# Performance work log

Hardware: AMD Instinct MI355X
Metric: run time of the kernel (lower is better)

The kernel has to match this reference:

```python
import jax, jax.numpy as jnp
import numpy as np
from jax import lax

B, N = 16, 4096


def _fps(xyz, npoint):
    # xyz: [N,3] -> [npoint] int32 indices (iterative farthest point sampling, start at idx 0)
    n = xyz.shape[0]
    def step(carry, _):
        dist, far = carry
        d = jnp.sum((xyz - xyz[far]) ** 2, axis=-1)
        dist = jnp.minimum(dist, d)
        nxt = jnp.argmax(dist).astype(jnp.int32)
        return (dist, nxt), far
    (_, _), idx = lax.scan(step, (jnp.full((n,), 1e10, xyz.dtype), jnp.int32(0)), None, length=npoint)
    return idx


def _ball_query(xyz, new_xyz, radius, nsample):
    # xyz: [N,3], new_xyz: [S,3] -> [S, nsample] neighbor indices within radius
    n = xyz.shape[0]
    sqr = jnp.sum((new_xyz[:, None, :] - xyz[None, :, :]) ** 2, axis=-1)  # [S,N]
    idx = jnp.where(sqr > radius * radius, n, jnp.arange(n)[None, :])
    idx = jnp.sort(idx, axis=-1)[:, :nsample]
    return jnp.where(idx == n, idx[:, :1], idx)  # pad misses with first hit


def _gather(p, i):
    return p[i]


def _mlp(feat, ws):
    # feat: [B,S,K,C]; 1x1 conv + folded eval-BN + ReLU per layer
    for W, b in ws:
        feat = jax.nn.relu(jnp.einsum('bskc,oc->bsko', feat, W) + b)
    return feat


def _sa(xyz, points, npoint, radius, nsample, ws):
    fps_idx = jax.vmap(_fps, in_axes=(0, None))(xyz, npoint)              # [B,S]
    new_xyz = jnp.take_along_axis(xyz, fps_idx[..., None], axis=1)         # [B,S,3]
    idx = jax.vmap(_ball_query, in_axes=(0, 0, None, None))(xyz, new_xyz, radius, nsample)  # [B,S,K]
    grouped_xyz = jax.vmap(_gather)(xyz, idx) - new_xyz[:, :, None, :]     # [B,S,K,3]
    if points is None:
        feat = grouped_xyz
    else:
        feat = jnp.concatenate([grouped_xyz, jax.vmap(_gather)(points, idx)], axis=-1)
    return new_xyz, jnp.max(_mlp(feat, ws), axis=2)                        # [B,S,Cout]


def _forward(x, ws1, ws2, ws3, fw, fb):
    b = x.shape[0]
    l1_xyz, l1_pts = _sa(x, None, 512, 0.2, 32, ws1)       # [B,512,3], [B,512,128]
    l2_xyz, l2_pts = _sa(l1_xyz, l1_pts, 128, 0.4, 64, ws2)  # [B,128,3], [B,128,256]
    feat = jnp.concatenate([l2_xyz, l2_pts], axis=-1)[:, None]  # group_all: [B,1,128,259]
    g = jnp.max(_mlp(feat, ws3), axis=2).reshape(b, 1024)
    return g @ fw.T + fb


_SPECS = [
    ('sa1_w0', (64, 3)), ('sa1_b0', (64,)), ('sa1_w1', (64, 64)), ('sa1_b1', (64,)), ('sa1_w2', (128, 64)), ('sa1_b2', (128,)),
    ('sa2_w0', (128, 131)), ('sa2_b0', (128,)), ('sa2_w1', (128, 128)), ('sa2_b1', (128,)), ('sa2_w2', (256, 128)), ('sa2_b2', (256,)),
    ('sa3_w0', (256, 259)), ('sa3_b0', (256,)), ('sa3_w1', (512, 256)), ('sa3_b1', (512,)), ('sa3_w2', (1024, 512)), ('sa3_b2', (1024,)),
    ('fw', (1024, 1024)), ('fb', (1024,)),
]


def setup_inputs() -> dict:
    key = jax.random.key(0)
    keys = jax.random.split(key, len(_SPECS) + 1)
    inp = {'x': jax.random.uniform(keys[0], (B, N, 3), dtype=jnp.float32)}
    for (name, shp), k in zip(_SPECS, keys[1:]):
        inp[name] = jax.random.normal(k, shp, dtype=jnp.float32) * 0.02
    return inp


def reference(x, sa1_w0, sa1_b0, sa1_w1, sa1_b1, sa1_w2, sa1_b2,
              sa2_w0, sa2_b0, sa2_w1, sa2_b1, sa2_w2, sa2_b2,
              sa3_w0, sa3_b0, sa3_w1, sa3_b1, sa3_w2, sa3_b2, fw, fb):
    ws1 = [(sa1_w0, sa1_b0), (sa1_w1, sa1_b1), (sa1_w2, sa1_b2)]
    ws2 = [(sa2_w0, sa2_b0), (sa2_w1, sa2_b1), (sa2_w2, sa2_b2)]
    ws3 = [(sa3_w0, sa3_b0), (sa3_w1, sa3_b1), (sa3_w2, sa3_b2)]
    return _forward(x, ws1, ws2, ws3, fw, fb)
```

## Files before the change

### kernel.cpp

```cpp
#include <hip/hip_runtime.h>

#ifndef BATCH
#define BATCH 16
#endif

typedef float f32x2 __attribute__((ext_vector_type(2)));
__device__ __forceinline__ f32x2 mk2(float a, float b) { f32x2 r; r.x = a; r.y = b; return r; }

template<int CTRL>
__device__ __forceinline__ float dppmaxf(float v)
{
    const int d = __builtin_amdgcn_update_dpp(__float_as_int(v), __float_as_int(v),
                                              CTRL, 0xf, 0xf, false);
    return fmaxf(v, __int_as_float(d));
}
template<int CTRL>
__device__ __forceinline__ unsigned dppminu(unsigned v)
{
    const unsigned d = (unsigned)__builtin_amdgcn_update_dpp((int)v, (int)v,
                                                             CTRL, 0xf, 0xf, false);
    return (d < v) ? d : v;
}
__device__ __forceinline__ float wave_max_bcast(float v)
{
    v = dppmaxf<0x111>(v);
    v = dppmaxf<0x112>(v);
    v = dppmaxf<0x114>(v);
    v = dppmaxf<0x118>(v);
    v = dppmaxf<0x142>(v);
    v = dppmaxf<0x143>(v);
    return __int_as_float(__builtin_amdgcn_readlane(__float_as_int(v), 63));
}
__device__ __forceinline__ unsigned wave_min_bcast(unsigned v)
{
    v = dppminu<0x111>(v);
    v = dppminu<0x112>(v);
    v = dppminu<0x114>(v);
    v = dppminu<0x118>(v);
    v = dppminu<0x142>(v);
    v = dppminu<0x143>(v);
    return (unsigned)__builtin_amdgcn_readlane((int)v, 63);
}

__device__ __forceinline__ void transpose_body(int blk, int tid,
    const float* __restrict__ s0, float* __restrict__ d0,
    const float* __restrict__ s1, float* __restrict__ d1,
    const float* __restrict__ s2, float* __restrict__ d2,
    const float* __restrict__ s3, float* __restrict__ d3,
    const float* __restrict__ s4, float* __restrict__ d4,
    const float* __restrict__ s5, float* __restrict__ d5,
    const float* __restrict__ s6, float* __restrict__ d6,
    const float* __restrict__ s7, float* __restrict__ d7,
    const float* __restrict__ s8, float* __restrict__ d8)
{
    int i = blk * 256 + tid;
    if (i < 192)    { d0[(i%3)  *64   + i/3  ] = s0[i]; return; }  i -= 192;
    if (i < 4096)   { d1[(i&63) *64   + (i>>6)] = s1[i]; return; } i -= 4096;
    if (i < 8192)   { d2[(i&63) *128  + (i>>6)] = s2[i]; return; } i -= 8192;
    if (i < 16768)  { d3[(i%131)*128  + i/131] = s3[i]; return; }  i -= 16768;
    if (i < 16384)  { d4[(i&127)*128  + (i>>7)] = s4[i]; return; } i -= 16384;
    if (i < 32768)  { d5[(i&127)*256  + (i>>7)] = s5[i]; return; } i -= 32768;
    if (i < 66304)  { d6[(i%259)*256  + i/259] = s6[i]; return; }  i -= 66304;
    if (i < 131072) { d7[(i&255)*512  + (i>>8)] = s7[i]; return; } i -= 131072;
    if (i < 524288) { d8[(i&511)*1024 + (i>>9)] = s8[i]; return; }
}

template<int N, int NP1, int NP2, int BLOCK>
__global__ __launch_bounds__(BLOCK)
void fps_fused(const float* __restrict__ xyz,
               float* __restrict__ out1, float* __restrict__ out2,
               const float* __restrict__ ts0, float* __restrict__ td0,
               const float* __restrict__ ts1, float* __restrict__ td1,
               const float* __restrict__ ts2, float* __restrict__ td2,
               const float* __restrict__ ts3, float* __restrict__ td3,
               const float* __restrict__ ts4, float* __restrict__ td4,
               const float* __restrict__ ts5, float* __restrict__ td5,
               const float* __restrict__ ts6, float* __restrict__ td6,
               const float* __restrict__ ts7, float* __restrict__ td7,
               const float* __restrict__ ts8, float* __restrict__ td8)
{
#pragma clang fp contract(off)
    if ((int)blockIdx.x >= BATCH) {
        transpose_body(blockIdx.x - BATCH, threadIdx.x,
                       ts0, td0, ts1, td1, ts2, td2, ts3, td3, ts4, td4,
                       ts5, td5, ts6, td6, ts7, td7, ts8, td8);
        return;
    }
    constexpr int P  = N / BLOCK;
    constexpr int P2 = NP1 / BLOCK;
    constexpr int NW = BLOCK / 64;
    __shared__ float sx[N], sy[N], sz[N];
    __shared__ float s2x[NP1], s2y[NP1], s2z[NP1];
    __shared__ float o2x[NP2], o2y[NP2], o2z[NP2];
    __shared__ unsigned long long wslot[2][NW];
    const int b = blockIdx.x, t = threadIdx.x;
    const int lane = t & 63, wv = t >> 6;
    const float* xb = xyz + (size_t)b * N * 3;
    float px[P], py[P], pz[P], dist[P];
#pragma unroll
    for (int j = 0; j < P; ++j) {
        const int i = t + j * BLOCK;
        const float x = xb[i*3+0], y = xb[i*3+1], z = xb[i*3+2];
        sx[i] = x; sy[i] = y; sz[i] = z;
        px[j] = x; py[j] = y; pz[j] = z;
        dist[j] = 1e10f;
    }
    __syncthreads();
    float fx = sx[0], fy = sy[0], fz = sz[0];
    if (t == 0) { s2x[0] = fx; s2y[0] = fy; s2z[0] = fz; }
    for (int s = 1; s < NP1; ++s) {
        float bestv = -1.f; int besti = 0;
#pragma unroll
        for (int j = 0; j < P; ++j) {
            const float dx = px[j]-fx, dy = py[j]-fy, dz = pz[j]-fz;
            const float d = (dx*dx + dy*dy) + dz*dz;
            const float nd = fminf(dist[j], d);
            dist[j] = nd;
            if (nd > bestv) { bestv = nd; besti = t + j * BLOCK; }
        }
        const float wm = wave_max_bcast(bestv);
        const unsigned cand = (bestv == wm) ? (unsigned)besti : 0xffffffffu;
        const unsigned wi = wave_min_bcast(cand);
        const int par = s & 1;
        if (lane == 0)
            wslot[par][wv] = ((unsigned long long)__float_as_uint(wm) << 32)
                           | (unsigned)(~wi);
        __syncthreads();
        unsigned long long pa = wslot[par][0];
#pragma unroll
        for (int w = 1; w < NW; ++w) {
            const unsigned long long pb = wslot[par][w];
            pa = (pb > pa) ? pb : pa;
        }
        const int far = (int)(~(unsigned)pa);
        fx = sx[far]; fy = sy[far]; fz = sz[far];
        if (t == 0) { s2x[s] = fx; s2y[s] = fy; s2z[s] = fz; }
    }
    __syncthreads();
    float mx[P2], my[P2], mz[P2], d2[P2];
#pragma unroll
    for (int j = 0; j < P2; ++j) {
        const int i = t + j * BLOCK;
        mx[j] = s2x[i]; my[j] = s2y[i]; mz[j] = s2z[i];
        d2[j] = 1e10f;
    }
    fx = s2x[0]; fy = s2y[0]; fz = s2z[0];
    if (t == 0) { o2x[0] = fx; o2y[0] = fy; o2z[0] = fz; }
    for (int s = 1; s < NP2; ++s) {
        float bestv = -1.f; int besti = 0;
#pragma unroll
        for (int j = 0; j < P2; ++j) {
            const float dx = mx[j]-fx, dy = my[j]-fy, dz = mz[j]-fz;
            const float d = (dx*dx + dy*dy) + dz*dz;
            const float nd = fminf(d2[j], d);
            d2[j] = nd;
            if (nd > bestv) { bestv = nd; besti = t + j * BLOCK; }
        }
        const float wm = wave_max_bcast(bestv);
        const unsigned cand = (bestv == wm) ? (unsigned)besti : 0xffffffffu;
        const unsigned wi = wave_min_bcast(cand);
        const int par = s & 1;
        if (lane == 0)
            wslot[par][wv] = ((unsigned long long)__float_as_uint(wm) << 32)
                           | (unsigned)(~wi);
        __syncthreads();
        unsigned long long pa = wslot[par][0];
#pragma unroll
        for (int w = 1; w < NW; ++w) {
            const unsigned long long pb = wslot[par][w];
            pa = (pb > pa) ? pb : pa;
        }
        const int far2 = (int)(~(unsigned)pa);
        fx = s2x[far2]; fy = s2y[far2]; fz = s2z[far2];
        if (t == 0) { o2x[s] = fx; o2y[s] = fy; o2z[s] = fz; }
    }
    __syncthreads();
    for (int i = t; i < NP1; i += BLOCK) {
        out1[((size_t)b*NP1 + i)*3 + 0] = s2x[i];
        out1[((size_t)b*NP1 + i)*3 + 1] = s2y[i];
        out1[((size_t)b*NP1 + i)*3 + 2] = s2z[i];
    }
    for (int i = t; i < NP2; i += BLOCK) {
        out2[((size_t)b*NP2 + i)*3 + 0] = o2x[i];
        out2[((size_t)b*NP2 + i)*3 + 1] = o2y[i];
        out2[((size_t)b*NP2 + i)*3 + 2] = o2z[i];
    }
}

template<int N, int S, int K>
__device__ __forceinline__ void ballq_body(const float* __restrict__ xyz,
                                           const float* __restrict__ nxyz,
                                           int* __restrict__ idx, const float r2,
                                           const int bid, const int tid)
{
#pragma clang fp contract(off)
    const int gw = (bid * 256 + tid) >> 6;
    const int lane = tid & 63;
    const int b = gw / S, s = gw % S;
    const float* xb = xyz + (size_t)b * N * 3;
    const float qx = nxyz[((size_t)b*S + s)*3 + 0];
    const float qy = nxyz[((size_t)b*S + s)*3 + 1];
    const float qz = nxyz[((size_t)b*S + s)*3 + 2];
    int* op = idx + ((size_t)b*S + s) * K;
    int base = 0, first = -1;
    for (int c = 0; c < N; c += 64) {
        const int i = c + lane;
        const float dx = xb[i*3+0]-qx, dy = xb[i*3+1]-qy, dz = xb[i*3+2]-qz;
        const float d = (dx*dx + dy*dy) + dz*dz;
        const bool hit = !(d > r2);
        const unsigned long long m = __ballot(hit);
        if (first < 0 && m) first = c + __builtin_ctzll(m);
        const int pos = base + __popcll(m & ((1ull << lane) - 1ull));
        if (hit && pos < K) op[pos] = i;
        base += __popcll(m);
        if (base >= K) break;
    }
    if (base < K && lane >= base && lane < K) op[lane] = first;
}

__global__ __launch_bounds__(256)
void ballq_both(const float* __restrict__ pts1, const float* __restrict__ q1,
                int* __restrict__ idx1, const float r2a,
                const float* __restrict__ pts2, const float* __restrict__ q2,
                int* __restrict__ idx2, const float r2b)
{
    const int nb1 = (BATCH * 512) / 4;
    if ((int)blockIdx.x < nb1)
        ballq_body<4096, 512, 32>(pts1, q1, idx1, r2a, blockIdx.x, threadIdx.x);
    else
        ballq_body<512, 128, 64>(pts2, q2, idx2, r2b, blockIdx.x - nb1, threadIdx.x);
}

__device__ __forceinline__ void fma16pk(f32x2 (&acc)[8], const float f,
                                        const float* __restrict__ wrow)
{
    const float4 w0 = ((const float4*)wrow)[0];
    const float4 w1 = ((const float4*)wrow)[1];
    const float4 w2 = ((const float4*)wrow)[2];
    const float4 w3 = ((const float4*)wrow)[3];
    const f32x2 ff = mk2(f, f);
    acc[0] += ff * mk2(w0.x, w0.y);
    acc[1] += ff * mk2(w0.z, w0.w);
    acc[2] += ff * mk2(w1.x, w1.y);
    acc[3] += ff * mk2(w1.z, w1.w);
    acc[4] += ff * mk2(w2.x, w2.y);
    acc[5] += ff * mk2(w2.z, w2.w);
    acc[6] += ff * mk2(w3.x, w3.y);
    acc[7] += ff * mk2(w3.z, w3.w);
}

__device__ __forceinline__ float pool_half(float v)
{
    v = fmaxf(v, __shfl_xor(v, 1));
    v = fmaxf(v, __shfl_xor(v, 2));
    v = fmaxf(v, __shfl_xor(v, 4));
    v = fmaxf(v, __shfl_xor(v, 8));
    v = fmaxf(v, __shfl_xor(v, 16));
    return v;
}
__device__ __forceinline__ float pool_full(float v)
{
    v = pool_half(v);
    return fmaxf(v, __shfl_xor(v, 32));
}

__global__ __launch_bounds__(256)
void sa1_fused(const float* __restrict__ xyz, const float* __restrict__ nxyz,
               const int* __restrict__ idx,
               const float* __restrict__ Wt0, const float* __restrict__ B0,
               const float* __restrict__ Wt1, const float* __restrict__ B1,
               const float* __restrict__ Wt2, const float* __restrict__ B2,
               float* __restrict__ out)
{
    __shared__ float buf[64][64];
    const int tid = threadIdx.x, lane = tid & 63;
    const int wave = __builtin_amdgcn_readfirstlane(tid >> 6);
    const int row0 = blockIdx.x * 64;
    const int myrow = row0 + lane;
    const int g = myrow >> 5, b = g >> 9;
    const int i = idx[myrow];
    const float* p = xyz + ((size_t)b*4096 + i) * 3;
    const float f0 = p[0] - nxyz[(size_t)g*3 + 0];
    const float f1 = p[1] - nxyz[(size_t)g*3 + 1];
    const float f2 = p[2] - nxyz[(size_t)g*3 + 2];
    const int oc0 = wave * 16;
    f32x2 aL[8], aH[8];
#pragma unroll
    for (int j = 0; j < 16; ++j) {
        const float v = B0[oc0+j] + f0*Wt0[0*64+oc0+j] + f1*Wt0[1*64+oc0+j] + f2*Wt0[2*64+oc0+j];
        buf[oc0+j][lane] = fmaxf(v, 0.f);
    }
    __syncthreads();
#pragma unroll
    for (int k = 0; k < 8; ++k) aL[k] = mk2(B1[oc0+2*k], B1[oc0+2*k+1]);
#pragma unroll 4
    for (int ci = 0; ci < 64; ++ci)
        fma16pk(aL, buf[ci][lane], Wt1 + ci*64 + oc0);
    __syncthreads();
#pragma unroll
    for (int k = 0; k < 8; ++k) {
        buf[oc0+2*k][lane]   = fmaxf(aL[k].x, 0.f);
        buf[oc0+2*k+1][lane] = fmaxf(aL[k].y, 0.f);
    }
    __syncthreads();
#pragma unroll
    for (int k = 0; k < 8; ++k) {
        aL[k] = mk2(B2[oc0+2*k], B2[oc0+2*k+1]);
        aH[k] = mk2(B2[64+oc0+2*k], B2[64+oc0+2*k+1]);
    }
#pragma unroll 2
    for (int ci = 0; ci < 64; ++ci) {
        const float f = buf[ci][lane];
        fma16pk(aL, f, Wt2 + ci*128 + oc0);
        fma16pk(aH, f, Wt2 + ci*128 + 64 + oc0);
    }
#pragma unroll
    for (int k = 0; k < 8; ++k) {
        const float v0 = pool_half(fmaxf(aL[k].x, 0.f));
        const float v1 = pool_half(fmaxf(aL[k].y, 0.f));
        const float w0 = pool_half(fmaxf(aH[k].x, 0.f));
        const float w1 = pool_half(fmaxf(aH[k].y, 0.f));
        if ((lane & 31) == 0) {
            const size_t orow = (size_t)((row0 + lane) >> 5) * 128;
            out[orow + oc0 + 2*k]       = v0;
            out[orow + oc0 + 2*k + 1]   = v1;
            out[orow + 64 + oc0 + 2*k]     = w0;
            out[orow + 64 + oc0 + 2*k + 1] = w1;
        }
    }
}

__global__ __launch_bounds__(256)
void sa2_fused(const float* __restrict__ l1xyz, const float* __restrict__ l1pts,
               const float* __restrict__ nxyz, const int* __restrict__ idx,
               const float* __restrict__ Wt0, const float* __restrict__ B0,
               const float* __restrict__ Wt1, const float* __restrict__ B1,
               const float* __restrict__ Wt2, const float* __restrict__ B2,
               float* __restrict__ out)
{
    __shared__ float buf[128][64];
    const int tid = threadIdx.x, lane = tid & 63;
    const int wave = __builtin_amdgcn_readfirstlane(tid >> 6);
    const int gblk = blockIdx.x;
    const int b = gblk >> 7;
    const int row0 = gblk * 64;
    const int myi = idx[row0 + lane];
    const float* pc = l1xyz + ((size_t)b*512 + myi) * 3;
    const float f0 = pc[0] - nxyz[(size_t)gblk*3 + 0];
    const float f1 = pc[1] - nxyz[(size_t)gblk*3 + 1];
    const float f2 = pc[2] - nxyz[(size_t)gblk*3 + 2];
    for (int r = wave; r < 64; r += 4) {
        const int i2 = idx[row0 + r];
        const float* src = l1pts + ((size_t)b*512 + i2) * 128;
        buf[lane][r ^ lane]    = src[lane];
        buf[lane+64][r ^ lane] = src[lane + 64];
    }
    __syncthreads();
    const int oc0 = wave * 16;
    f32x2 aL[8], aH[8];
#pragma unroll
    for (int k = 0; k < 8; ++k) {
        const int j0 = oc0 + 2*k, j1 = oc0 + 2*k + 1;
        aL[k] = mk2(B0[j0]    + f0*Wt0[j0]     + f1*Wt0[128+j0]    + f2*Wt0[256+j0],
                    B0[j1]    + f0*Wt0[j1]     + f1*Wt0[128+j1]    + f2*Wt0[256+j1]);
        aH[k] = mk2(B0[64+j0] + f0*Wt0[64+j0]  + f1*Wt0[192+j0]    + f2*Wt0[320+j0],
                    B0[64+j1] + f0*Wt0[64+j1]  + f1*Wt0[192+j1]    + f2*Wt0[320+j1]);
    }
#pragma unroll 2
    for (int ci = 0; ci < 128; ++ci) {
        const float f = buf[ci][lane ^ (ci & 63)];
        const float* wp = Wt0 + (size_t)(ci+3)*128;
        fma16pk(aL, f, wp + oc0);
        fma16pk(aH, f, wp + 64 + oc0);
    }
    __syncthreads();
#pragma unroll
    for (int k = 0; k < 8; ++k) {
        buf[oc0+2*k][lane]      = fmaxf(aL[k].x, 0.f);
        buf[oc0+2*k+1][lane]    = fmaxf(aL[k].y, 0.f);
        buf[64+oc0+2*k][lane]   = fmaxf(aH[k].x, 0.f);
        buf[64+oc0+2*k+1][lane] = fmaxf(aH[k].y, 0.f);
    }
    __syncthreads();
#pragma unroll
    for (int k = 0; k < 8; ++k) {
        aL[k] = mk2(B1[oc0+2*k], B1[oc0+2*k+1]);
        aH[k] = mk2(B1[64+oc0+2*k], B1[64+oc0+2*k+1]);
    }
#pragma unroll 2
    for (int ci = 0; ci < 128; ++ci) {
        const float f = buf[ci][lane];
        const float* wp = Wt1 + (size_t)ci*128;
        fma16pk(aL, f, wp + oc0);
        fma16pk(aH, f, wp + 64 + oc0);
    }
    __syncthreads();
#pragma unroll
    for (int k = 0; k < 8; ++k) {
        buf[oc0+2*k][lane]      = fmaxf(aL[k].x, 0.f);
        buf[oc0+2*k+1][lane]    = fmaxf(aL[k].y, 0.f);
        buf[64+oc0+2*k][lane]   = fmaxf(aH[k].x, 0.f);
        buf[64+oc0+2*k+1][lane] = fmaxf(aH[k].y, 0.f);
    }
    __syncthreads();
    float* orow = out + (size_t)gblk * 256;
    for (int half = 0; half < 2; ++half) {
        const int oc = half*128 + oc0;
#pragma unroll
        for (int k = 0; k < 8; ++k) {
            aL[k] = mk2(B2[oc+2*k], B2[oc+2*k+1]);
            aH[k] = mk2(B2[64+oc+2*k], B2[64+oc+2*k+1]);
        }
#pragma unroll 2
        for (int ci = 0; ci < 128; ++ci) {
            const float f = buf[ci][lane];
            const float* wp = Wt2 + (size_t)ci*256;
            fma16pk(aL, f, wp + oc);
            fma16pk(aH, f, wp + 64 + oc);
        }
#pragma unroll
        for (int k = 0; k < 8; ++k) {
            const float v0 = pool_full(fmaxf(aL[k].x, 0.f));
            const float v1 = pool_full(fmaxf(aL[k].y, 0.f));
            const float w0 = pool_full(fmaxf(aH[k].x, 0.f));
            const float w1 = pool_full(fmaxf(aH[k].y, 0.f));
            if (lane == 0) {
                orow[oc + 2*k]        = v0;
                orow[oc + 2*k + 1]    = v1;
                orow[64 + oc + 2*k]   = w0;
                orow[64 + oc + 2*k+1] = w1;
            }
        }
    }
}

template<int CIN, int COUT, bool CONCAT3, bool POOL>
__global__ __launch_bounds__(256)
void mlp_gemm_kernel(const float* __restrict__ inA, const float* __restrict__ inB,
                     const float* __restrict__ Wt, const float* __restrict__ Bb,
                     float* __restrict__ out)
{
    __shared__ float featS[128][64];
    const int tid = threadIdx.x, lane = tid & 63;
    const int wave = __builtin_amdgcn_readfirstlane(tid >> 6);
    const int row0 = blockIdx.x * 64;
    const int oc0 = blockIdx.y * 64 + wave * 16;
    f32x2 acc[8];
#pragma unroll
    for (int k = 0; k < 8; ++k) acc[k] = mk2(Bb[oc0+2*k], Bb[oc0+2*k+1]);
    for (int c0 = 0; c0 < CIN; c0 += 128) {
        const int csz = (CIN - c0 < 128) ? (CIN - c0) : 128;
        __syncthreads();
        for (int r = wave; r < 64; r += 4) {
            const int row = row0 + r;
            for (int cl = lane; cl < csz; cl += 64) {
                const int cig = c0 + cl;
                float v;
                if (CONCAT3)
                    v = (cig < 3) ? inA[(size_t)row*3 + cig]
                                  : inB[(size_t)row*(CIN-3) + (cig - 3)];
                else
                    v = inA[(size_t)row*CIN + cig];
                featS[cl][r ^ (cl & 63)] = v;
            }
        }
        __syncthreads();
        if (csz == 128) {
#pragma unroll 4
            for (int ci = 0; ci < 128; ++ci)
                fma16pk(acc, featS[ci][lane ^ (ci & 63)], Wt + (size_t)(c0+ci)*COUT + oc0);
        } else {
            for (int ci = 0; ci < csz; ++ci)
                fma16pk(acc, featS[ci][lane ^ (ci & 63)], Wt + (size_t)(c0+ci)*COUT + oc0);
        }
    }
    if (POOL) {
#pragma unroll
        for (int k = 0; k < 8; ++k) {
            const float v0 = pool_full(fmaxf(acc[k].x, 0.f));
            const float v1 = pool_full(fmaxf(acc[k].y, 0.f));
            if (lane == 0) {
                out[(size_t)blockIdx.x * COUT + oc0 + 2*k]     = v0;
                out[(size_t)blockIdx.x * COUT + oc0 + 2*k + 1] = v1;
            }
        }
    } else {
        float4 o0, o1, o2, o3;
        o0.x=fmaxf(acc[0].x,0.f); o0.y=fmaxf(acc[0].y,0.f); o0.z=fmaxf(acc[1].x,0.f); o0.w=fmaxf(acc[1].y,0.f);
        o1.x=fmaxf(acc[2].x,0.f); o1.y=fmaxf(acc[2].y,0.f); o1.z=fmaxf(acc[3].x,0.f); o1.w=fmaxf(acc[3].y,0.f);
        o2.x=fmaxf(acc[4].x,0.f); o2.y=fmaxf(acc[4].y,0.f); o2.z=fmaxf(acc[5].x,0.f); o2.w=fmaxf(acc[5].y,0.f);
        o3.x=fmaxf(acc[6].x,0.f); o3.y=fmaxf(acc[6].y,0.f); o3.z=fmaxf(acc[7].x,0.f); o3.w=fmaxf(acc[7].y,0.f);
        float4* op = (float4*)(out + (size_t)(row0 + lane)*COUT + oc0);
        op[0]=o0; op[1]=o1; op[2]=o2; op[3]=o3;
    }
}

__global__ __launch_bounds__(256)
void fc_kernel(const float* __restrict__ pmax, const float* __restrict__ fw,
               const float* __restrict__ fb, float* __restrict__ y)
{
    const int gw = (blockIdx.x * 256 + threadIdx.x) >> 6;
    const int lane = threadIdx.x & 63;
    const int b = gw >> 10, o = gw & 1023;
    const float4* g0 = (const float4*)(pmax + (size_t)(2*b) * 1024);
    const float4* g1 = (const float4*)(pmax + (size_t)(2*b+1) * 1024);
    const float4* wv = (const float4*)(fw + (size_t)o * 1024);
    float acc = 0.f;
#pragma unroll
    for (int r = 0; r < 4; ++r) {
        const float4 a = g0[lane + r*64];
        const float4 c = g1[lane + r*64];
        const float4 w = wv[lane + r*64];
        acc += fmaxf(a.x,c.x)*w.x + fmaxf(a.y,c.y)*w.y
             + fmaxf(a.z,c.z)*w.z + fmaxf(a.w,c.w)*w.w;
    }
#pragma unroll
    for (int m = 32; m >= 1; m >>= 1) acc += __shfl_xor(acc, m);
    if (lane == 0) y[gw] = acc + fb[o];
}

extern "C" void kernel_launch(void* const* d_in, const int* in_sizes, int n_in,
                              void* d_out, int out_size, void* d_ws, size_t ws_size,
                              hipStream_t stream)
{
    (void)in_sizes; (void)n_in; (void)out_size; (void)ws_size;
    const float* x   = (const float*)d_in[0];
    const float* s1w0 = (const float*)d_in[1];  const float* s1b0 = (const float*)d_in[2];
    const float* s1w1 = (const float*)d_in[3];  const float* s1b1 = (const float*)d_in[4];
    const float* s1w2 = (const float*)d_in[5];  const float* s1b2 = (const float*)d_in[6];
    const float* s2w0 = (const float*)d_in[7];  const float* s2b0 = (const float*)d_in[8];
    const float* s2w1 = (const float*)d_in[9];  const float* s2b1 = (const float*)d_in[10];
    const float* s2w2 = (const float*)d_in[11]; const float* s2b2 = (const float*)d_in[12];
    const float* s3w0 = (const float*)d_in[13]; const float* s3b0 = (const float*)d_in[14];
    const float* s3w1 = (const float*)d_in[15]; const float* s3b1 = (const float*)d_in[16];
    const float* s3w2 = (const float*)d_in[17]; const float* s3b2 = (const float*)d_in[18];
    const float* fw  = (const float*)d_in[19]; const float* fb  = (const float*)d_in[20];
    float* y = (float*)d_out;

    char* ws = (char*)d_ws;
    float* l1_xyz = (float*)(ws + 0);
    int*   idx1   = (int*)  (ws + 98304);
    float* l1_pts = (float*)(ws + 1146880);
    float* l2_xyz = (float*)(ws + 5341184);
    int*   idx2   = (int*)  (ws + 5365760);
    float* l2_pts = (float*)(ws + 5890048);
    float* h1     = (float*)(ws + 7987200);
    float* h2     = (float*)(ws + 10084352);
    float* pmax   = (float*)(ws + 14278656);
    float* wt1_0  = (float*)(ws + 14409728);
    float* wt1_1  = (float*)(ws + 14410496);
    float* wt1_2  = (float*)(ws + 14426880);
    float* wt2_0  = (float*)(ws + 14459648);
    float* wt2_1  = (float*)(ws + 14526720);
    float* wt2_2  = (float*)(ws + 14592256);
    float* wt3_0  = (float*)(ws + 14723328);
    float* wt3_1  = (float*)(ws + 14988544);
    float* wt3_2  = (float*)(ws + 15512832);

    const float r2_1 = (float)(0.2 * 0.2);
    const float r2_2 = (float)(0.4 * 0.4);

    fps_fused<4096, 512, 128, 256><<<BATCH + 3126, 256, 0, stream>>>(
        x, l1_xyz, l2_xyz,
        s1w0, wt1_0, s1w1, wt1_1, s1w2, wt1_2,
        s2w0, wt2_0, s2w1, wt2_1, s2w2, wt2_2,
        s3w0, wt3_0, s3w1, wt3_1, s3w2, wt3_2);
    ballq_both<<<(BATCH*512)/4 + (BATCH*128)/4, 256, 0, stream>>>(
        x, l1_xyz, idx1, r2_1, l1_xyz, l2_xyz, idx2, r2_2);
    sa1_fused<<<(BATCH*512*32)/64, 256, 0, stream>>>(x, l1_xyz, idx1,
        wt1_0, s1b0, wt1_1, s1b1, wt1_2, s1b2, l1_pts);
    sa2_fused<<<BATCH*128, 256, 0, stream>>>(l1_xyz, l1_pts, l2_xyz, idx2,
        wt2_0, s2b0, wt2_1, s2b1, wt2_2, s2b2, l2_pts);
    mlp_gemm_kernel<259, 256,  true,  false><<<dim3(32, 4),  256, 0, stream>>>(l2_xyz, l2_pts, wt3_0, s3b0, h1);
    mlp_gemm_kernel<256, 512,  false, false><<<dim3(32, 8),  256, 0, stream>>>(h1, nullptr, wt3_1, s3b1, h2);
    mlp_gemm_kernel<512, 1024, false, true ><<<dim3(32, 16), 256, 0, stream>>>(h2, nullptr, wt3_2, s3b2, pmax);
    fc_kernel<<<(BATCH*1024)/4, 256, 0, stream>>>(pmax, fw, fb, y);
}
```

Measured before the change: 928.0 us.

## Compute SA1 MLP fully in registers per point, removing shared-memory staging

The SA1 fused MLP is restructured so each thread owns one grouped point and computes all 64/64/128 channels of the three layers in registers. Previously the four waves split output channels and exchanged activations through a shared buffer with block barriers. The new kernel removes LDS traffic and syncthreads, and each block now covers 256 rows instead of 64. In exchange it needs about 128 live floats plus accumulators per thread, which raises register pressure and lowers occupancy. Each thread also reads every weight row, where before it read only its wave's slice.

Measured after the change: 1.457 ms. 57.0% more time.

```diff
diff --git a/kernel.cpp b/kernel.cpp
--- a/kernel.cpp
+++ b/kernel.cpp
@@ -265,67 +265,60 @@
 }
 
 __global__ __launch_bounds__(256)
-void sa1_fused(const float* __restrict__ xyz, const float* __restrict__ nxyz,
-               const int* __restrict__ idx,
-               const float* __restrict__ Wt0, const float* __restrict__ B0,
-               const float* __restrict__ Wt1, const float* __restrict__ B1,
-               const float* __restrict__ Wt2, const float* __restrict__ B2,
-               float* __restrict__ out)
-{
-    __shared__ float buf[64][64];
+void sa1_reg(const float* __restrict__ xyz, const float* __restrict__ nxyz,
+             const int* __restrict__ idx,
+             const float* __restrict__ Wt0, const float* __restrict__ B0,
+             const float* __restrict__ Wt1, const float* __restrict__ B1,
+             const float* __restrict__ Wt2, const float* __restrict__ B2,
+             float* __restrict__ out)
+{
     const int tid = threadIdx.x, lane = tid & 63;
     const int wave = __builtin_amdgcn_readfirstlane(tid >> 6);
-    const int row0 = blockIdx.x * 64;
-    const int myrow = row0 + lane;
+    const int myrow = blockIdx.x * 256 + wave * 64 + lane;
     const int g = myrow >> 5, b = g >> 9;
     const int i = idx[myrow];
     const float* p = xyz + ((size_t)b*4096 + i) * 3;
     const float f0 = p[0] - nxyz[(size_t)g*3 + 0];
     const float f1 = p[1] - nxyz[(size_t)g*3 + 1];
     const float f2 = p[2] - nxyz[(size_t)g*3 + 2];
-    const int oc0 = wave * 16;
-    f32x2 aL[8], aH[8];
-#pragma unroll
-    for (int j = 0; j < 16; ++j) {
-        const float v = B0[oc0+j] + f0*Wt0[0*64+oc0+j] + f1*Wt0[1*64+oc0+j] + f2*Wt0[2*64+oc0+j];
-        buf[oc0+j][lane] = fmaxf(v, 0.f);
-    }
-    __syncthreads();
-#pragma unroll
-    for (int k = 0; k < 8; ++k) aL[k] = mk2(B1[oc0+2*k], B1[oc0+2*k+1]);
-#pragma unroll 4
-    for (int ci = 0; ci < 64; ++ci)
-        fma16pk(aL, buf[ci][lane], Wt1 + ci*64 + oc0);
-    __syncthreads();
-#pragma unroll
-    for (int k = 0; k < 8; ++k) {
-        buf[oc0+2*k][lane]   = fmaxf(aL[k].x, 0.f);
-        buf[oc0+2*k+1][lane] = fmaxf(aL[k].y, 0.f);
-    }
-    __syncthreads();
-#pragma unroll
-    for (int k = 0; k < 8; ++k) {
-        aL[k] = mk2(B2[oc0+2*k], B2[oc0+2*k+1]);
-        aH[k] = mk2(B2[64+oc0+2*k], B2[64+oc0+2*k+1]);
-    }
-#pragma unroll 2
-    for (int ci = 0; ci < 64; ++ci) {
-        const float f = buf[ci][lane];
-        fma16pk(aL, f, Wt2 + ci*128 + oc0);
-        fma16pk(aH, f, Wt2 + ci*128 + 64 + oc0);
-    }
-#pragma unroll
-    for (int k = 0; k < 8; ++k) {
-        const float v0 = pool_half(fmaxf(aL[k].x, 0.f));
-        const float v1 = pool_half(fmaxf(aL[k].y, 0.f));
-        const float w0 = pool_half(fmaxf(aH[k].x, 0.f));
-        const float w1 = pool_half(fmaxf(aH[k].y, 0.f));
-        if ((lane & 31) == 0) {
-            const size_t orow = (size_t)((row0 + lane) >> 5) * 128;
-            out[orow + oc0 + 2*k]       = v0;
-            out[orow + oc0 + 2*k + 1]   = v1;
-            out[orow + 64 + oc0 + 2*k]     = w0;
-            out[orow + 64 + oc0 + 2*k + 1] = w1;
+    float h1[64];
+#pragma unroll
+    for (int oc = 0; oc < 64; ++oc)
+        h1[oc] = fmaxf(B0[oc] + f0*Wt0[0*64+oc] + f1*Wt0[1*64+oc] + f2*Wt0[2*64+oc], 0.f);
+    float h2[64];
+#pragma unroll
+    for (int ch = 0; ch < 4; ++ch) {
+        const int oc0 = ch * 16;
+        f32x2 acc[8];
+#pragma unroll
+        for (int k = 0; k < 8; ++k) acc[k] = mk2(B1[oc0+2*k], B1[oc0+2*k+1]);
+#pragma unroll
+        for (int ci = 0; ci < 64; ++ci)
+            fma16pk(acc, h1[ci], Wt1 + ci*64 + oc0);
+#pragma unroll
+        for (int k = 0; k < 8; ++k) {
+            h2[oc0+2*k]   = fmaxf(acc[k].x, 0.f);
+            h2[oc0+2*k+1] = fmaxf(acc[k].y, 0.f);
+        }
+    }
+    const size_t orow = (size_t)g * 128;
+#pragma unroll
+    for (int ch = 0; ch < 8; ++ch) {
+        const int oc0 = ch * 16;
+        f32x2 acc[8];
+#pragma unroll
+        for (int k = 0; k < 8; ++k) acc[k] = mk2(B2[oc0+2*k], B2[oc0+2*k+1]);
+#pragma unroll
+        for (int ci = 0; ci < 64; ++ci)
+            fma16pk(acc, h2[ci], Wt2 + ci*128 + oc0);
+#pragma unroll
+        for (int k = 0; k < 8; ++k) {
+            const float v0 = pool_half(fmaxf(acc[k].x, 0.f));
+            const float v1 = pool_half(fmaxf(acc[k].y, 0.f));
+            if ((lane & 31) == 0) {
+                out[orow + ((lane >> 5) ? 0 : 0) + oc0 + 2*k]     = v0;
+                out[orow + oc0 + 2*k + 1] = v1;
+            }
         }
     }
 }
@@ -567,7 +560,7 @@
         s3w0, wt3_0, s3w1, wt3_1, s3w2, wt3_2);
     ballq_both<<<(BATCH*512)/4 + (BATCH*128)/4, 256, 0, stream>>>(
         x, l1_xyz, idx1, r2_1, l1_xyz, l2_xyz, idx2, r2_2);
-    sa1_fused<<<(BATCH*512*32)/64, 256, 0, stream>>>(x, l1_xyz, idx1,
+    sa1_reg<<<(BATCH*512*32)/256, 256, 0, stream>>>(x, l1_xyz, idx1,
         wt1_0, s1b0, wt1_1, s1b1, wt1_2, s1b2, l1_pts);
     sa2_fused<<<BATCH*128, 256, 0, stream>>>(l1_xyz, l1_pts, l2_xyz, idx2,
         wt2_0, s2b0, wt2_1, s2b1, wt2_2, s2b2, l2_pts);
```
